# Performance work log

Hardware: AMD Instinct MI355X
Metric: run time of the kernel (lower is better)

The kernel has to match this reference:

```python
import jax, jax.numpy as jnp
import numpy as np

# relation r = 2*i + j over node types i (dst) and j (src); 4 relations total
J_OF_R = np.array([0, 1, 0, 1])  # source node-type per relation


def spmm_layer(H, rows, cols, vals, W):
    """Multi-relational GCN layer.
    H: [2, N, d_in] node features per type; rows/cols/vals: [4, E] COO adjacencies;
    W: [4, d_in, d_out]. Returns [2, N, d_out] (pre-activation, summed over j).
    """
    N = H.shape[1]
    Hj = H[jnp.asarray(J_OF_R)]                      # [4, N, d_in] source feats per relation
    XW = jnp.einsum('rnd,rde->rne', Hj, W)           # dense transform per relation

    def one_rel(r, c, v, x):
        # sparse A @ (H W): gather src rows, scale by edge val, scatter-add to dst
        return jax.ops.segment_sum(v[:, None] * x[c], r, num_segments=N)

    msgs = jax.vmap(one_rel)(rows, cols, vals, XW)   # [4, N, d_out]
    # add_n over source types j for each destination type i
    return jnp.stack([msgs[0] + msgs[1], msgs[2] + msgs[3]])


def setup_inputs() -> dict:
    key = jax.random.key(0)
    ks = jax.random.split(key, 11)
    N, F, E, H = 50000, 128, 500000, 64
    s = 0.1  # weight init scale to keep activations stable over 4 layers
    return {
        'feat': jax.random.normal(ks[0], (2, N, F), jnp.float32),
        'adj1_rows': jax.random.randint(ks[1], (4, E), 0, N),
        'adj1_cols': jax.random.randint(ks[2], (4, E), 0, N),
        'adj1_vals': jax.random.uniform(ks[3], (4, E), jnp.float32),
        'adj2_rows': jax.random.randint(ks[4], (4, E), 0, N),
        'adj2_cols': jax.random.randint(ks[5], (4, E), 0, N),
        'adj2_vals': jax.random.uniform(ks[6], (4, E), jnp.float32),
        'W1': jax.random.normal(ks[7], (4, F, H), jnp.float32) * s,
        'W2': jax.random.normal(ks[8], (4, H, H), jnp.float32) * s,
        'W3': jax.random.normal(ks[9], (4, H, H), jnp.float32) * s,
        'W4': jax.random.normal(ks[10], (4, H, H), jnp.float32) * s,
    }


def reference(feat, adj1_rows, adj1_cols, adj1_vals,
              adj2_rows, adj2_cols, adj2_vals, W1, W2, W3, W4):
    # external embed: two sparse multi-relational GCN layers on adj_mats1
    h = jax.nn.relu(spmm_layer(feat, adj1_rows, adj1_cols, adj1_vals, W1))
    h = jax.nn.relu(spmm_layer(h, adj1_rows, adj1_cols, adj1_vals, W2))
    # inner embed: two layers on adj_mats2; final embeddings have no ReLU (add_n only)
    h = jax.nn.relu(spmm_layer(h, adj2_rows, adj2_cols, adj2_vals, W3))
    emb = spmm_layer(h, adj2_rows, adj2_cols, adj2_vals, W4)
    return emb  # [2, N, 64] node embeddings per object type
```

## Files before the change

kernel.cpp:

```cpp
#include <hip/hip_runtime.h>
#include <hip/hip_bf16.h>


#define DOUT 64
#define WBINS 12800
#define CCH   8

typedef __attribute__((ext_vector_type(8))) short s16x8;
typedef __attribute__((ext_vector_type(4))) float f32x4;

__device__ __forceinline__ float bf2f_lo(unsigned u) {
    return __uint_as_float(u << 16);
}
__device__ __forceinline__ float bf2f_hi(unsigned u) {
    return __uint_as_float(u & 0xffff0000u);
}
__device__ __forceinline__ short f2bf(float x) {
    union { __hip_bfloat16 h; short s; } u;
    u.h = __float2bfloat16(x);
    return u.s;
}

__global__ __launch_bounds__(1024) void k_build(
    const int* __restrict__ rows1, const int* __restrict__ rows2,
    int E, int chunkE, int N, int* __restrict__ cnt3, unsigned short* __restrict__ rank)
{
    __shared__ int bins[WBINS];
    const int w = blockIdx.x;
    const int s = blockIdx.y;
    const int c = blockIdx.z;
    const int lo = w * WBINS;
    const int hi = min(N, lo + WBINS);
    const int nb = hi - lo;
    if (nb <= 0) return;
    const int* rows = (s < 4) ? rows1 : rows2;
    const size_t base = (size_t)(s & 3) * E;
    const int e0 = c * chunkE;
    const int e1 = min(E, e0 + chunkE);

    for (int b = threadIdx.x; b < nb; b += 1024) bins[b] = 0;
    __syncthreads();

    for (int e = e0 + threadIdx.x; e < e1; e += 1024) {
        const int row = rows[base + e];
        if (row >= lo && row < hi) {
            const int r = atomicAdd(&bins[row - lo], 1);
            rank[(size_t)s * E + e] = (unsigned short)r;
        }
    }
    __syncthreads();

    for (int b = threadIdx.x; b < nb; b += 1024)
        cnt3[((size_t)(s * CCH + c)) * N + lo + b] = bins[b];
}

__global__ __launch_bounds__(256) void k_rowsum(
    int* __restrict__ cnt3, int* __restrict__ cnt, int N)
{
    const int row = blockIdx.x * 256 + threadIdx.x;
    const int s   = blockIdx.y;
    if (row >= N) return;
    int sum = 0;
#pragma unroll
    for (int c = 0; c < CCH; ++c) {
        const size_t idx = ((size_t)(s * CCH + c)) * N + row;
        const int v = cnt3[idx];
        cnt3[idx] = sum;
        sum += v;
    }
    cnt[(size_t)s * N + row] = sum;
}

__global__ __launch_bounds__(256) void k_scan1(
    const int* __restrict__ cnt, int M, int* __restrict__ out, int* __restrict__ partials)
{
    __shared__ int sm[256];
    const int i = blockIdx.x * 256 + threadIdx.x;
    const int x = (i < M) ? cnt[i] : 0;
    sm[threadIdx.x] = x;
    __syncthreads();
    for (int off = 1; off < 256; off <<= 1) {
        int t = (threadIdx.x >= off) ? sm[threadIdx.x - off] : 0;
        __syncthreads();
        sm[threadIdx.x] += t;
        __syncthreads();
    }
    if (i < M) out[i] = sm[threadIdx.x] - x;
    if (threadIdx.x == 255) partials[blockIdx.x] = sm[255];
}

__global__ __launch_bounds__(256) void k_scan2(int* __restrict__ partials, int nb)
{
    __shared__ int sm[256];
    __shared__ int carry_s;
    if (threadIdx.x == 0) carry_s = 0;
    __syncthreads();
    for (int base = 0; base < nb; base += 256) {
        const int i = base + threadIdx.x;
        const int x = (i < nb) ? partials[i] : 0;
        sm[threadIdx.x] = x;
        __syncthreads();
        for (int off = 1; off < 256; off <<= 1) {
            int t = (threadIdx.x >= off) ? sm[threadIdx.x - off] : 0;
            __syncthreads();
            sm[threadIdx.x] += t;
            __syncthreads();
        }
        const int carry = carry_s;
        const int incl  = sm[threadIdx.x];
        __syncthreads();
        if (i < nb) partials[i] = incl - x + carry;
        if (threadIdx.x == 255) carry_s = carry + incl;
        __syncthreads();
    }
}

__global__ __launch_bounds__(256) void k_scan3(
    int* __restrict__ row_ptr, const int* __restrict__ partials, int M, int total)
{
    const int i = blockIdx.x * 256 + threadIdx.x;
    if (i < M) row_ptr[i] += partials[blockIdx.x];
    if (i == 0) row_ptr[M] = total;
}

__global__ __launch_bounds__(256) void k_base(
    int* __restrict__ cnt3, const int* __restrict__ row_ptr, int N)
{
    const int row = blockIdx.x * 256 + threadIdx.x;
    const int s   = blockIdx.y;
    const int c   = blockIdx.z;
    if (row >= N) return;
    cnt3[((size_t)(s * CCH + c)) * N + row] += row_ptr[(size_t)s * N + row];
}

__global__ __launch_bounds__(256) void k_fill(
    const int* __restrict__ rows1, const int* __restrict__ cols1, const float* __restrict__ vals1,
    const int* __restrict__ rows2, const int* __restrict__ cols2, const float* __restrict__ vals2,
    int E, int chunkE, int N,
    const int* __restrict__ base3, const unsigned short* __restrict__ rank,
    int2* __restrict__ cv)
{
    const int s  = blockIdx.x;
    const int z  = blockIdx.z;
    const int c  = z % CCH;
    const int wf = z / CCH;
    const int lo = wf * WBINS;
    const int hi = min(N, lo + WBINS);
    const int el = blockIdx.y * 256 + threadIdx.x;
    const int e  = c * chunkE + el;
    if (el >= chunkE || e >= E) return;
    const int* rows   = (s < 4) ? rows1 : rows2;
    const size_t idx  = (size_t)(s & 3) * E + e;
    const int row = rows[idx];
    if (row < lo || row >= hi) return;
    const int* cols   = (s < 4) ? cols1 : cols2;
    const float* vals = (s < 4) ? vals1 : vals2;
    const int pos = base3[((size_t)(s * CCH + c)) * N + row]
                  + (int)rank[(size_t)s * E + e];
    cv[pos] = make_int2(cols[idx], __float_as_int(vals[idx]));
}

__global__ __launch_bounds__(256) void k_wprep(
    const float* __restrict__ W, short* __restrict__ wb, int d_in)
{
    const int KS  = d_in >> 5;
    const int tid = blockIdx.x * 256 + threadIdx.x;
    if (tid >= 2 * 8 * KS * 64) return;
    const int l    = tid & 63;
    const int rest = tid >> 6;
    const int ks   = rest % KS;
    const int tt   = rest / KS;
    const int t    = tt & 7;
    const int j    = tt >> 3;
    const int r    = ((t >> 2) << 1) + j;
    const int c    = ((t & 3) << 4) + (l & 15);
    const int k0   = (ks << 5) + ((l >> 4) << 3);
    s16x8 v;
#pragma unroll
    for (int e = 0; e < 8; ++e)
        v[e] = f2bf(W[((size_t)r * d_in + k0 + e) * 64 + c]);
    *reinterpret_cast<s16x8*>(wb + (size_t)tid * 8) = v;
}

template<int KS>
__global__ __launch_bounds__(256) void k_gemm(
    const float* __restrict__ H,
    const short* __restrict__ wb,
    __hip_bfloat16* __restrict__ XW,
    int N)
{
    __shared__ __hip_bfloat16 lds_o[64][136];
    const int d_in = KS * 32;
    const int j    = blockIdx.y;
    const int wv   = threadIdx.x >> 6;
    const int lane = threadIdx.x & 63;
    const int row0 = blockIdx.x * 64;

    const int arow = row0 + wv * 16 + (lane & 15);
    const int rc   = (arow < N) ? arow : (N - 1);
    const float* Hb = H + (size_t)j * N * d_in + (size_t)rc * d_in + ((lane >> 4) << 3);

    s16x8 a[KS];
#pragma unroll
    for (int ks = 0; ks < KS; ++ks) {
        union { float4 v; float f[4]; } f0, f1;
        f0.v = *reinterpret_cast<const float4*>(Hb + ks * 32);
        f1.v = *reinterpret_cast<const float4*>(Hb + ks * 32 + 4);
        s16x8 t;
#pragma unroll
        for (int e = 0; e < 4; ++e) { t[e] = f2bf(f0.f[e]); t[4 + e] = f2bf(f1.f[e]); }
        a[ks] = t;
    }

    f32x4 acc[8];
#pragma unroll
    for (int nt = 0; nt < 8; ++nt) acc[nt] = (f32x4){0.f, 0.f, 0.f, 0.f};

    const short* wbase = wb + ((size_t)j * 8 * KS * 64 + lane) * 8;
#pragma unroll
    for (int ks = 0; ks < KS; ++ks) {
#pragma unroll
        for (int nt = 0; nt < 8; ++nt) {
            const s16x8 b = *reinterpret_cast<const s16x8*>(
                wbase + (size_t)(nt * KS + ks) * 64 * 8);
            acc[nt] = __builtin_amdgcn_mfma_f32_16x16x32_bf16(a[ks], b, acc[nt], 0, 0, 0);
        }
    }

#pragma unroll
    for (int nt = 0; nt < 8; ++nt)
#pragma unroll
        for (int r = 0; r < 4; ++r)
            lds_o[wv * 16 + ((lane >> 4) << 2) + r][nt * 16 + (lane & 15)] =
                __float2bfloat16(acc[nt][r]);
    __syncthreads();

    const int t = threadIdx.x;
#pragma unroll
    for (int p = 0; p < 4; ++p) {
        const int r = p * 16 + (t >> 4);
        const int n = row0 + r;
        if (n < N) {
            const int g = t & 15;
            const uint4 v = *reinterpret_cast<const uint4*>(&lds_o[r][g * 8]);
            *reinterpret_cast<uint4*>(
                (unsigned short*)XW + ((size_t)(j * 2 + (g >> 3)) * N + n) * 64 + (g & 7) * 8) = v;
        }
    }
}

template<int RELU>
__global__ __launch_bounds__(256) void k_spmm(
    const int* __restrict__ row_ptr, int set4,
    const int2* __restrict__ cv,
    const unsigned short* __restrict__ XW,
    float* __restrict__ out,
    int N)
{
    const int i    = blockIdx.y;
    const int wv   = threadIdx.x >> 6;
    const int n    = blockIdx.x * 4 + wv;
    if (n >= N) return;
    const int lane = threadIdx.x & 63;
    const int slot = lane >> 3;
    const int ol   = lane & 7;

    float acc[8];
#pragma unroll
    for (int k = 0; k < 8; ++k) acc[k] = 0.f;

#pragma unroll
    for (int js = 0; js < 2; ++js) {
        const int seg = set4 + 2 * i + js;
        const int* rp = row_ptr + (size_t)seg * N;
        const int s = rp[n];
        const int e = rp[n + 1];
        const unsigned short* xw = XW + ((size_t)(js * 2 + i) * N) * 64 + ol * 8;

        for (int t0 = s; t0 < e; t0 += 8) {
            const int t  = t0 + slot;
            const bool v = (t < e);
            const int tc = v ? t : (e - 1);
            const int2 p = cv[tc];
            const float val = v ? __int_as_float(p.y) : 0.f;
            const uint4 u = *reinterpret_cast<const uint4*>(xw + ((size_t)p.x << 6));
            acc[0] = fmaf(val, bf2f_lo(u.x), acc[0]);
            acc[1] = fmaf(val, bf2f_hi(u.x), acc[1]);
            acc[2] = fmaf(val, bf2f_lo(u.y), acc[2]);
            acc[3] = fmaf(val, bf2f_hi(u.y), acc[3]);
            acc[4] = fmaf(val, bf2f_lo(u.z), acc[4]);
            acc[5] = fmaf(val, bf2f_hi(u.z), acc[5]);
            acc[6] = fmaf(val, bf2f_lo(u.w), acc[6]);
            acc[7] = fmaf(val, bf2f_hi(u.w), acc[7]);
        }
    }

#pragma unroll
    for (int m = 8; m < 64; m <<= 1) {
#pragma unroll
        for (int k = 0; k < 8; ++k) acc[k] += __shfl_xor(acc[k], m, 64);
    }

    if (slot == 0) {
        if (RELU) {
#pragma unroll
            for (int k = 0; k < 8; ++k) acc[k] = fmaxf(acc[k], 0.f);
        }
        float* op = out + ((size_t)i * N + n) * DOUT + ol * 8;
        *reinterpret_cast<float4*>(op)     = make_float4(acc[0], acc[1], acc[2], acc[3]);
        *reinterpret_cast<float4*>(op + 4) = make_float4(acc[4], acc[5], acc[6], acc[7]);
    }
}

extern "C" void kernel_launch(void* const* d_in, const int* in_sizes, int n_in,
                              void* d_out, int out_size, void* d_ws, size_t ws_size,
                              hipStream_t stream) {
    const float* feat      = (const float*)d_in[0];
    const int*   adj1_rows = (const int*)  d_in[1];
    const int*   adj1_cols = (const int*)  d_in[2];
    const float* adj1_vals = (const float*)d_in[3];
    const int*   adj2_rows = (const int*)  d_in[4];
    const int*   adj2_cols = (const int*)  d_in[5];
    const float* adj2_vals = (const float*)d_in[6];
    const float* W1        = (const float*)d_in[7];
    const float* W2        = (const float*)d_in[8];
    const float* W3        = (const float*)d_in[9];
    const float* W4        = (const float*)d_in[10];

    const int E = in_sizes[1] / 4;
    const int F = in_sizes[7] / (4 * DOUT);
    const int N = in_sizes[0] / (2 * F);
    const int M = 8 * N;
    const int nb1 = (M + 255) / 256;
    const int nw  = (N + WBINS - 1) / WBINS;
    const int chunkE = (E + CCH - 1) / CCH;

    auto align256 = [](size_t x) { return (x + 255) & ~(size_t)255; };

    const size_t cv_b   = align256((size_t)8 * E * sizeof(int2));
    const size_t rp_b   = align256(((size_t)M + 8) * sizeof(int));
    const size_t xw_b   = align256((size_t)2 * 2 * N * 64 * sizeof(__hip_bfloat16));
    const size_t ha_b   = align256((size_t)2 * N * DOUT * sizeof(float));

    char* w = (char*)d_ws;
    int2* cv      = (int2*)w;  w += cv_b;
    int*  row_ptr = (int*)w;   w += rp_b;
    __hip_bfloat16* XW = (__hip_bfloat16*)w;
    int*  cnt3    = (int*)w;   w += xw_b;
    float* Ha     = (float*)w; w += ha_b;
    unsigned short* rank = (unsigned short*)Ha;
    int*  cnt     = (int*)((char*)Ha + align256((size_t)8 * E * sizeof(unsigned short)));
    int*  partials= (int*)((char*)cnt + align256((size_t)M * sizeof(int)));
    short* wb1    = (short*)w;
    short* wb2    = wb1 + 32768;
    short* wb3    = wb2 + 16384;
    short* wb4    = wb3 + 16384;
    float* out    = (float*)d_out;

    k_wprep<<<16, 256, 0, stream>>>(W1, wb1, F);
    k_wprep<<<8, 256, 0, stream>>>(W2, wb2, DOUT);
    k_wprep<<<8, 256, 0, stream>>>(W3, wb3, DOUT);
    k_wprep<<<8, 256, 0, stream>>>(W4, wb4, DOUT);

    k_build<<<dim3(nw, 8, CCH), 1024, 0, stream>>>(adj1_rows, adj2_rows, E, chunkE, N, cnt3, rank);
    k_rowsum<<<dim3((N + 255) / 256, 8), 256, 0, stream>>>(cnt3, cnt, N);
    k_scan1<<<nb1, 256, 0, stream>>>(cnt, M, row_ptr, partials);
    k_scan2<<<1, 256, 0, stream>>>(partials, nb1);
    k_scan3<<<nb1, 256, 0, stream>>>(row_ptr, partials, M, 8 * E);
    k_base<<<dim3((N + 255) / 256, 8, CCH), 256, 0, stream>>>(cnt3, row_ptr, N);
    k_fill<<<dim3(8, (chunkE + 255) / 256, CCH * nw), 256, 0, stream>>>(
        adj1_rows, adj1_cols, adj1_vals, adj2_rows, adj2_cols, adj2_vals,
        E, chunkE, N, cnt3, rank, cv);

    const dim3 ggrid((N + 63) / 64, 2);
    const dim3 sgrid((N + 3) / 4, 2);

    auto layer = [&](const float* Hin, int d_in, const short* wbl,
                     int set4, float* Hout, int relu_out) {
        if (d_in == 128) k_gemm<4><<<ggrid, 256, 0, stream>>>(Hin, wbl, XW, N);
        else             k_gemm<2><<<ggrid, 256, 0, stream>>>(Hin, wbl, XW, N);
        if (relu_out)
            k_spmm<1><<<sgrid, 256, 0, stream>>>(row_ptr, set4, cv,
                                                 (const unsigned short*)XW, Hout, N);
        else
            k_spmm<0><<<sgrid, 256, 0, stream>>>(row_ptr, set4, cv,
                                                 (const unsigned short*)XW, Hout, N);
    };

    layer(feat, F,    wb1, 0, Ha,  1);
    layer(Ha,   DOUT, wb2, 0, out, 1);
    layer(out,  DOUT, wb3, 4, Ha,  1);
    layer(Ha,   DOUT, wb4, 4, out, 0);
}
```

Before: 398.6 us.

## Split SpMM into per-relation half-width blocks and defer add/ReLU into GEMM

Re-lays out XW as eight 32-column slices (relation × column half) so each SpMM block gathers 64-byte rows from a smaller working set, which should improve cache locality. When enough workspace is available, each (relation, half) pair runs as its own block. One source relation writes fp32 output and the other writes a bf16 partial buffer, so the separate relations no longer accumulate in the same block. The sum of the two relations and the ReLU move into the next GEMM's A-load, plus a final add kernel for the last layer. This adds bf16 rounding of one partial sum and an extra final pass, and it relies on ws_size being large enough to take the split path.

```diff
diff --git a/kernel.cpp b/kernel.cpp
--- a/kernel.cpp
+++ b/kernel.cpp
@@ -15,8 +15,8 @@
 __device__ __forceinline__ float bf2f_hi(unsigned u) {
     return __uint_as_float(u & 0xffff0000u);
 }
-__device__ __forceinline__ short f2bf(float x) {
-    union { __hip_bfloat16 h; short s; } u;
+__device__ __forceinline__ unsigned short f2bf(float x) {
+    union { __hip_bfloat16 h; unsigned short s; } u;
     u.h = __float2bfloat16(x);
     return u.s;
 }
@@ -178,15 +178,16 @@
     s16x8 v;
 #pragma unroll
     for (int e = 0; e < 8; ++e)
-        v[e] = f2bf(W[((size_t)r * d_in + k0 + e) * 64 + c]);
+        v[e] = (short)f2bf(W[((size_t)r * d_in + k0 + e) * 64 + c]);
     *reinterpret_cast<s16x8*>(wb + (size_t)tid * 8) = v;
 }
 
-template<int KS>
+template<int KS, int MODE>
 __global__ __launch_bounds__(256) void k_gemm(
     const float* __restrict__ H,
+    const unsigned short* __restrict__ P,
     const short* __restrict__ wb,
-    __hip_bfloat16* __restrict__ XW,
+    unsigned short* __restrict__ XWs,
     int N)
 {
     __shared__ __hip_bfloat16 lds_o[64][136];
@@ -198,7 +199,9 @@
 
     const int arow = row0 + wv * 16 + (lane & 15);
     const int rc   = (arow < N) ? arow : (N - 1);
-    const float* Hb = H + (size_t)j * N * d_in + (size_t)rc * d_in + ((lane >> 4) << 3);
+    const int koff = (lane >> 4) << 3;
+    const float* Hb = H + (size_t)j * N * d_in + (size_t)rc * d_in + koff;
+    const unsigned short* Pb = P + ((size_t)j * N + rc) * DOUT + koff;
 
     s16x8 a[KS];
 #pragma unroll
@@ -206,9 +209,22 @@
         union { float4 v; float f[4]; } f0, f1;
         f0.v = *reinterpret_cast<const float4*>(Hb + ks * 32);
         f1.v = *reinterpret_cast<const float4*>(Hb + ks * 32 + 4);
+        float pv[8];
+        if (MODE == 2) {
+            const uint4 pu = *reinterpret_cast<const uint4*>(Pb + ks * 32);
+            pv[0] = bf2f_lo(pu.x); pv[1] = bf2f_hi(pu.x);
+            pv[2] = bf2f_lo(pu.y); pv[3] = bf2f_hi(pu.y);
+            pv[4] = bf2f_lo(pu.z); pv[5] = bf2f_hi(pu.z);
+            pv[6] = bf2f_lo(pu.w); pv[7] = bf2f_hi(pu.w);
+        }
         s16x8 t;
 #pragma unroll
-        for (int e = 0; e < 4; ++e) { t[e] = f2bf(f0.f[e]); t[4 + e] = f2bf(f1.f[e]); }
+        for (int e = 0; e < 4; ++e) {
+            float v0 = f0.f[e], v1 = f1.f[e];
+            if (MODE == 2) { v0 += pv[e]; v1 += pv[4 + e]; }
+            if (MODE >= 1) { v0 = fmaxf(v0, 0.f); v1 = fmaxf(v1, 0.f); }
+            t[e] = (short)f2bf(v0); t[4 + e] = (short)f2bf(v1);
+        }
         a[ks] = t;
     }
 
@@ -242,19 +258,90 @@
         const int n = row0 + r;
         if (n < N) {
             const int g = t & 15;
+            const int q = (j << 2) | ((g >> 3) << 1) | ((g >> 2) & 1);
             const uint4 v = *reinterpret_cast<const uint4*>(&lds_o[r][g * 8]);
             *reinterpret_cast<uint4*>(
-                (unsigned short*)XW + ((size_t)(j * 2 + (g >> 3)) * N + n) * 64 + (g & 7) * 8) = v;
-        }
-    }
-}
-
-template<int RELU>
-__global__ __launch_bounds__(256) void k_spmm(
+                XWs + ((size_t)q * N + n) * 32 + (g & 3) * 8) = v;
+        }
+    }
+}
+
+__global__ __launch_bounds__(256) void k_spmm_split(
     const int* __restrict__ row_ptr, int set4,
     const int2* __restrict__ cv,
-    const unsigned short* __restrict__ XW,
-    float* __restrict__ out,
+    const unsigned short* __restrict__ XWs,
+    float* __restrict__ outF,
+    unsigned short* __restrict__ Pb,
+    int N)
+{
+    const int bid  = blockIdx.x;
+    const int q    = bid & 7;
+    const int wv   = threadIdx.x >> 6;
+    const int n    = (bid >> 3) * 4 + wv;
+    if (n >= N) return;
+    const int lane = threadIdx.x & 63;
+    const int slot = lane >> 3;
+    const int ol   = lane & 7;
+    const int js   = q >> 2, i = (q >> 1) & 1, half = q & 1;
+
+    const int* rp = row_ptr + (size_t)(set4 + 2 * i + js) * N;
+    const int s = rp[n];
+    const int e = rp[n + 1];
+
+    const unsigned short* xw = XWs + ((size_t)q * N) * 32 + ol * 4;
+
+    float a0 = 0.f, a1 = 0.f, a2 = 0.f, a3 = 0.f;
+    for (int t0 = s; t0 < e; t0 += 8) {
+        const int t  = t0 + slot;
+        const bool v = (t < e);
+        const int tc = v ? t : (e - 1);
+        const int2 p = cv[tc];
+        const float val = v ? __int_as_float(p.y) : 0.f;
+        const uint2 u = *reinterpret_cast<const uint2*>(xw + ((size_t)p.x << 5));
+        a0 = fmaf(val, bf2f_lo(u.x), a0);
+        a1 = fmaf(val, bf2f_hi(u.x), a1);
+        a2 = fmaf(val, bf2f_lo(u.y), a2);
+        a3 = fmaf(val, bf2f_hi(u.y), a3);
+    }
+
+#pragma unroll
+    for (int m = 8; m < 64; m <<= 1) {
+        a0 += __shfl_xor(a0, m, 64);
+        a1 += __shfl_xor(a1, m, 64);
+        a2 += __shfl_xor(a2, m, 64);
+        a3 += __shfl_xor(a3, m, 64);
+    }
+
+    if (slot == 0) {
+        const size_t off = ((size_t)i * N + n) * DOUT + half * 32 + ol * 4;
+        if (js == 0) {
+            *reinterpret_cast<float4*>(outF + off) = make_float4(a0, a1, a2, a3);
+        } else {
+            uint2 pk;
+            pk.x = (unsigned)f2bf(a0) | ((unsigned)f2bf(a1) << 16);
+            pk.y = (unsigned)f2bf(a2) | ((unsigned)f2bf(a3) << 16);
+            *reinterpret_cast<uint2*>(Pb + off) = pk;
+        }
+    }
+}
+
+__global__ __launch_bounds__(256) void k_addP(
+    float* __restrict__ outF, const unsigned short* __restrict__ Pb, int total4)
+{
+    const int t = blockIdx.x * 256 + threadIdx.x;
+    if (t >= total4) return;
+    const uint2 pu = *reinterpret_cast<const uint2*>(Pb + (size_t)t * 4);
+    float4 o = *reinterpret_cast<const float4*>(outF + (size_t)t * 4);
+    o.x += bf2f_lo(pu.x); o.y += bf2f_hi(pu.x);
+    o.z += bf2f_lo(pu.y); o.w += bf2f_hi(pu.y);
+    *reinterpret_cast<float4*>(outF + (size_t)t * 4) = o;
+}
+
+__global__ __launch_bounds__(256) void k_spmm_whole(
+    const int* __restrict__ row_ptr, int set4,
+    const int2* __restrict__ cv,
+    const unsigned short* __restrict__ XWs,
+    float* __restrict__ outF,
     int N)
 {
     const int i    = blockIdx.y;
@@ -271,11 +358,11 @@
 
 #pragma unroll
     for (int js = 0; js < 2; ++js) {
-        const int seg = set4 + 2 * i + js;
-        const int* rp = row_ptr + (size_t)seg * N;
+        const int* rp = row_ptr + (size_t)(set4 + 2 * i + js) * N;
         const int s = rp[n];
         const int e = rp[n + 1];
-        const unsigned short* xw = XW + ((size_t)(js * 2 + i) * N) * 64 + ol * 8;
+        const int q = (js << 2) | (i << 1) | (ol >> 2);
+        const unsigned short* xw = XWs + ((size_t)q * N) * 32 + (ol & 3) * 8;
 
         for (int t0 = s; t0 < e; t0 += 8) {
             const int t  = t0 + slot;
@@ -283,7 +370,7 @@
             const int tc = v ? t : (e - 1);
             const int2 p = cv[tc];
             const float val = v ? __int_as_float(p.y) : 0.f;
-            const uint4 u = *reinterpret_cast<const uint4*>(xw + ((size_t)p.x << 6));
+            const uint4 u = *reinterpret_cast<const uint4*>(xw + ((size_t)p.x << 5));
             acc[0] = fmaf(val, bf2f_lo(u.x), acc[0]);
             acc[1] = fmaf(val, bf2f_hi(u.x), acc[1]);
             acc[2] = fmaf(val, bf2f_lo(u.y), acc[2]);
@@ -302,11 +389,7 @@
     }
 
     if (slot == 0) {
-        if (RELU) {
-#pragma unroll
-            for (int k = 0; k < 8; ++k) acc[k] = fmaxf(acc[k], 0.f);
-        }
-        float* op = out + ((size_t)i * N + n) * DOUT + ol * 8;
+        float* op = outF + ((size_t)i * N + n) * DOUT + ol * 8;
         *reinterpret_cast<float4*>(op)     = make_float4(acc[0], acc[1], acc[2], acc[3]);
         *reinterpret_cast<float4*>(op + 4) = make_float4(acc[4], acc[5], acc[6], acc[7]);
     }
@@ -337,24 +420,29 @@
 
     auto align256 = [](size_t x) { return (x + 255) & ~(size_t)255; };
 
-    const size_t cv_b   = align256((size_t)8 * E * sizeof(int2));
-    const size_t rp_b   = align256(((size_t)M + 8) * sizeof(int));
-    const size_t xw_b   = align256((size_t)2 * 2 * N * 64 * sizeof(__hip_bfloat16));
-    const size_t ha_b   = align256((size_t)2 * N * DOUT * sizeof(float));
+    const size_t cv_b  = align256((size_t)8 * E * sizeof(int2));
+    const size_t rp_b  = align256(((size_t)M + 8) * sizeof(int));
+    const size_t xw_b  = align256((size_t)8 * N * 32 * sizeof(unsigned short));
+    const size_t ha_b  = align256((size_t)2 * N * DOUT * sizeof(float));
+    const size_t wb_b  = align256(65536) + 3 * align256(32768);
+    const size_t p_b   = align256((size_t)2 * N * DOUT * sizeof(unsigned short));
+
+    const int big = (ws_size >= cv_b + rp_b + xw_b + ha_b + wb_b + p_b) ? 1 : 0;
 
     char* w = (char*)d_ws;
     int2* cv      = (int2*)w;  w += cv_b;
     int*  row_ptr = (int*)w;   w += rp_b;
-    __hip_bfloat16* XW = (__hip_bfloat16*)w;
+    unsigned short* XWs = (unsigned short*)w;
     int*  cnt3    = (int*)w;   w += xw_b;
     float* Ha     = (float*)w; w += ha_b;
     unsigned short* rank = (unsigned short*)Ha;
     int*  cnt     = (int*)((char*)Ha + align256((size_t)8 * E * sizeof(unsigned short)));
     int*  partials= (int*)((char*)cnt + align256((size_t)M * sizeof(int)));
-    short* wb1    = (short*)w;
-    short* wb2    = wb1 + 32768;
-    short* wb3    = wb2 + 16384;
-    short* wb4    = wb3 + 16384;
+    short* wb1    = (short*)w; w += align256(65536);
+    short* wb2    = (short*)w; w += align256(32768);
+    short* wb3    = (short*)w; w += align256(32768);
+    short* wb4    = (short*)w; w += align256(32768);
+    unsigned short* P = (unsigned short*)w;
     float* out    = (float*)d_out;
 
     k_wprep<<<16, 256, 0, stream>>>(W1, wb1, F);
@@ -373,22 +461,37 @@
         E, chunkE, N, cnt3, rank, cv);
 
     const dim3 ggrid((N + 63) / 64, 2);
-    const dim3 sgrid((N + 3) / 4, 2);
-
-    auto layer = [&](const float* Hin, int d_in, const short* wbl,
-                     int set4, float* Hout, int relu_out) {
-        if (d_in == 128) k_gemm<4><<<ggrid, 256, 0, stream>>>(Hin, wbl, XW, N);
-        else             k_gemm<2><<<ggrid, 256, 0, stream>>>(Hin, wbl, XW, N);
-        if (relu_out)
-            k_spmm<1><<<sgrid, 256, 0, stream>>>(row_ptr, set4, cv,
-                                                 (const unsigned short*)XW, Hout, N);
-        else
-            k_spmm<0><<<sgrid, 256, 0, stream>>>(row_ptr, set4, cv,
-                                                 (const unsigned short*)XW, Hout, N);
+    const int  sblocks_split = 8 * ((N + 3) / 4);
+    const dim3 sgrid_whole((N + 3) / 4, 2);
+
+    auto gemmL = [&](const float* Hin, int mode, int ks, const short* wbl) {
+        if (ks == 4) {
+            k_gemm<4, 0><<<ggrid, 256, 0, stream>>>(Hin, P, wbl, XWs, N);
+        } else if (mode == 2) {
+            k_gemm<2, 2><<<ggrid, 256, 0, stream>>>(Hin, P, wbl, XWs, N);
+        } else {
+            k_gemm<2, 1><<<ggrid, 256, 0, stream>>>(Hin, P, wbl, XWs, N);
+        }
     };
 
-    layer(feat, F,    wb1, 0, Ha,  1);
-    layer(Ha,   DOUT, wb2, 0, out, 1);
-    layer(out,  DOUT, wb3, 4, Ha,  1);
-    layer(Ha,   DOUT, wb4, 4, out, 0);
-}
+    if (big) {
+        gemmL(feat, 0, 4, wb1);
+        k_spmm_split<<<sblocks_split, 256, 0, stream>>>(row_ptr, 0, cv, XWs, Ha, P, N);
+        gemmL(Ha, 2, 2, wb2);
+        k_spmm_split<<<sblocks_split, 256, 0, stream>>>(row_ptr, 0, cv, XWs, out, P, N);
+        gemmL(out, 2, 2, wb3);
+        k_spmm_split<<<sblocks_split, 256, 0, stream>>>(row_ptr, 4, cv, XWs, Ha, P, N);
+        gemmL(Ha, 2, 2, wb4);
+        k_spmm_split<<<sblocks_split, 256, 0, stream>>>(row_ptr, 4, cv, XWs, out, P, N);
+        k_addP<<<(2 * N * DOUT / 4 + 255) / 256, 256, 0, stream>>>(out, P, 2 * N * DOUT / 4);
+    } else {
+        gemmL(feat, 0, 4, wb1);
+        k_spmm_whole<<<sgrid_whole, 256, 0, stream>>>(row_ptr, 0, cv, XWs, Ha, N);
+        gemmL(Ha, 1, 2, wb2);
+        k_spmm_whole<<<sgrid_whole, 256, 0, stream>>>(row_ptr, 0, cv, XWs, out, N);
+        gemmL(out, 1, 2, wb3);
+        k_spmm_whole<<<sgrid_whole, 256, 0, stream>>>(row_ptr, 4, cv, XWs, Ha, N);
+        gemmL(Ha, 1, 2, wb4);
+        k_spmm_whole<<<sgrid_whole, 256, 0, stream>>>(row_ptr, 4, cv, XWs, out, N);
+    }
+}
```

After: 613.1 us. 1.54x slower.
